# Performance work log

Hardware: AMD Instinct MI355X
Metric: run time of the kernel (lower is better)

The kernel has to match this reference:

```python
import jax, jax.numpy as jnp
import numpy as np

EMBED_DIM = 1024
NUM_HEADS = 16
HEAD_DIM = EMBED_DIM // NUM_HEADS
SCALE = float(np.sqrt(HEAD_DIM))
B, TQ, TK = 2, 2048, 2048


def setup_inputs() -> dict:
    key = jax.random.key(0)
    ks = jax.random.split(key, 16)
    s = 1.0 / np.sqrt(EMBED_DIM)
    inp = {
        "query": jax.random.normal(ks[0], (B, TQ, EMBED_DIM), jnp.float32),
        "key": jax.random.normal(ks[1], (B, TK, EMBED_DIM), jnp.float32),
        "value": jax.random.normal(ks[2], (B, TK, EMBED_DIM), jnp.float32),
        "key_padding_mask": jnp.zeros((B, TK), dtype=bool),
        "Wq": jax.random.uniform(ks[3], (EMBED_DIM, EMBED_DIM), jnp.float32, -s, s),
        "bq": jax.random.uniform(ks[4], (EMBED_DIM,), jnp.float32, -s, s),
        "Wk": jax.random.uniform(ks[5], (EMBED_DIM, EMBED_DIM), jnp.float32, -s, s),
        "bk": jax.random.uniform(ks[6], (EMBED_DIM,), jnp.float32, -s, s),
        "Wv": jax.random.uniform(ks[7], (EMBED_DIM, EMBED_DIM), jnp.float32, -s, s),
        "bv": jax.random.uniform(ks[8], (EMBED_DIM,), jnp.float32, -s, s),
        "Wo": jax.random.uniform(ks[9], (EMBED_DIM, EMBED_DIM), jnp.float32, -s, s),
        "bo": jax.random.uniform(ks[10], (EMBED_DIM,), jnp.float32, -s, s),
        "clr_bias_q": jax.random.normal(ks[11], (NUM_HEADS, 1, HEAD_DIM), jnp.float32) * 0.02,
        "clr_bias_k": jax.random.normal(ks[12], (NUM_HEADS, 1, HEAD_DIM), jnp.float32) * 0.02,
    }
    return inp


def reference(query, key, value, key_padding_mask, Wq, bq, Wk, bk, Wv, bv, Wo, bo,
              clr_bias_q, clr_bias_k):
    Bsz, Tq, _ = query.shape
    Tk = key.shape[1]

    def split_heads(x, W, b, T):
        # Linear (torch convention: x @ W.T + b) then [B, H, T, Dh]
        y = jnp.einsum('bte,fe->btf', x, W) + b
        return y.reshape(Bsz, T, NUM_HEADS, HEAD_DIM).transpose(0, 2, 1, 3)

    q = split_heads(query, Wq, bq, Tq)   # [B,H,Tq,Dh]
    k = split_heads(key, Wk, bk, Tk)     # [B,H,Tk,Dh]
    v = split_heads(value, Wv, bv, Tk)   # [B,H,Tk,Dh]

    # CLR centering + learned bias (Aitchison similarity)
    q_c = q - jnp.mean(q, axis=-1, keepdims=True) + clr_bias_q[None]
    k_c = k - jnp.mean(k, axis=-1, keepdims=True) + clr_bias_k[None]
    scores = jnp.einsum('bhqd,bhkd->bhqk', q_c, k_c) / SCALE  # [B,H,Tq,Tk]

    mask = key_padding_mask[:, None, None, :]  # [B,1,1,Tk], True = ignore
    scores = jnp.where(mask, -jnp.inf, scores)

    attn = jax.nn.softmax(scores, axis=-1)
    out = jnp.einsum('bhqk,bhkd->bhqd', attn, v)
    out = out.transpose(0, 2, 1, 3).reshape(Bsz, Tq, EMBED_DIM)
    return jnp.einsum('bte,fe->btf', out, Wo) + bo
```

## Files before the change

### kernel.cpp

```cpp
#include <hip/hip_runtime.h>
#include <stdint.h>

static constexpr int EMB   = 1024;
static constexpr int HEADS = 16;
static constexpr int HD    = 64;
static constexpr int BATCH = 2;
static constexpr int SEQ   = 2048;
static constexpr int BT    = BATCH * SEQ;
static constexpr float QSC = 0.18033688011112042f;

typedef short   short8  __attribute__((ext_vector_type(8)));
typedef float   float4v __attribute__((ext_vector_type(4)));

__device__ __forceinline__ ushort f2bf(float f) {
    union { float f; uint32_t i; } v; v.f = f;
    uint32_t x = v.i;
    return (ushort)((x + 0x7FFFu + ((x >> 16) & 1u)) >> 16);
}
__device__ __forceinline__ ushort f2bf_rn(float f) {
    union { float f; uint32_t i; } v; v.f = f;
    return (ushort)((v.i + 0x8000u) >> 16);
}
__device__ __forceinline__ uint32_t pack2bf(float lo, float hi) {
    union { float f; uint32_t u; } a, b; a.f = lo; b.f = hi;
    uint32_t ra = a.u + 0x7FFFu + ((a.u >> 16) & 1u);
    uint32_t rb = b.u + 0x7FFFu + ((b.u >> 16) & 1u);
    return (rb & 0xFFFF0000u) | (ra >> 16);
}
__device__ __forceinline__ float fast_exp2(float x) {
#if __has_builtin(__builtin_amdgcn_exp2f)
    return __builtin_amdgcn_exp2f(x);
#else
    return exp2f(x);
#endif
}

__device__ __forceinline__ void async_ld16(const void* g, void* l) {
    __builtin_amdgcn_global_load_lds(
        (const __attribute__((address_space(1))) void*)g,
        (__attribute__((address_space(3))) void*)l,
        16, 0, 0);
}

__global__ void cvt_all(const float* __restrict__ q, const float* __restrict__ k,
                        const float* __restrict__ v,
                        const float* __restrict__ wq, const float* __restrict__ wk,
                        const float* __restrict__ wv, const float* __restrict__ wo,
                        ushort* __restrict__ qb, ushort* __restrict__ kb,
                        ushort* __restrict__ vb,
                        ushort* __restrict__ wqb, ushort* __restrict__ wkb,
                        ushort* __restrict__ wvb, ushort* __restrict__ wob)
{
    int bid = blockIdx.x;
    const float* src; ushort* dst; size_t off;
    if (bid < 6144) {
        int seg = bid >> 11;
        src = seg == 0 ? q : (seg == 1 ? k : v);
        dst = seg == 0 ? qb : (seg == 1 ? kb : vb);
        off = (size_t)(bid & 2047) * 2048;
    } else {
        int t = bid - 6144, seg = t >> 9;
        src = seg == 0 ? wq : (seg == 1 ? wk : (seg == 2 ? wv : wo));
        dst = seg == 0 ? wqb : (seg == 1 ? wkb : (seg == 2 ? wvb : wob));
        off = (size_t)(t & 511) * 2048;
    }
    size_t base = off + (size_t)threadIdx.x * 8;
    float4 a0 = *(const float4*)(src + base);
    float4 a1 = *(const float4*)(src + base + 4);
    uint32_t o[4] = { pack2bf(a0.x, a0.y), pack2bf(a0.z, a0.w),
                      pack2bf(a1.x, a1.y), pack2bf(a1.z, a1.w) };
    *(uint4*)(dst + base) = *(uint4*)o;
}

__device__ __forceinline__ void gemm_core_128(
    const ushort* __restrict__ A, const ushort* __restrict__ W,
    int m0, int n0, int K,
    ushort* As, ushort* Ws,
    int wid, int lane, float4v acc[4][4])
{
    const int lrow8 = lane >> 3;
    const int gc    = (lane & 7) ^ lrow8;
    const ushort* Ab = A + (size_t)m0 * K + gc * 8;
    const ushort* Wb = W + (size_t)n0 * K + gc * 8;
    const int wm = (wid >> 1) * 64;
    const int wn = (wid & 1) * 64;

    for (int k0 = 0; k0 < K; k0 += 64) {
        __syncthreads();
#pragma unroll
        for (int it = 0; it < 4; ++it) {
            int rg = it * 4 + wid;
            int row = rg * 8 + lrow8;
            async_ld16(Ab + (size_t)row * K + k0, &As[rg * 512]);
            async_ld16(Wb + (size_t)row * K + k0, &Ws[rg * 512]);
        }
        __syncthreads();
#pragma unroll
        for (int ks = 0; ks < 2; ++ks) {
            const int c = ks * 4 + (lane >> 4);
            short8 af[4], wf[4];
#pragma unroll
            for (int i = 0; i < 4; i++) {
                int row = wm + i * 16 + (lane & 15);
                af[i] = *(const short8*)&As[row * 64 + ((c ^ (row & 7)) * 8)];
            }
#pragma unroll
            for (int j = 0; j < 4; j++) {
                int row = wn + j * 16 + (lane & 15);
                wf[j] = *(const short8*)&Ws[row * 64 + ((c ^ (row & 7)) * 8)];
            }
#pragma unroll
            for (int i = 0; i < 4; i++)
#pragma unroll
                for (int j = 0; j < 4; j++)
                    acc[i][j] = __builtin_amdgcn_mfma_f32_16x16x32_bf16(af[i], wf[j], acc[i][j], 0, 0, 0);
        }
    }
}

__global__ __launch_bounds__(256, 3)
void gemm_qkv(const ushort* __restrict__ qb, const ushort* __restrict__ kb,
              const ushort* __restrict__ vb,
              const ushort* __restrict__ wqb, const ushort* __restrict__ wkb,
              const ushort* __restrict__ wvb,
              const float* __restrict__ bq, const float* __restrict__ bk,
              const float* __restrict__ bv,
              const float* __restrict__ cbq, const float* __restrict__ cbk,
              ushort* __restrict__ qc, ushort* __restrict__ kc,
              ushort* __restrict__ vt)
{
    constexpr int SST = 136;
    __shared__ __align__(16) ushort S[128 * SST];

    const int z = blockIdx.z;
    const ushort* A    = z == 0 ? qb  : (z == 1 ? kb  : vb);
    const ushort* W    = z == 0 ? wqb : (z == 1 ? wkb : wvb);
    const float*  bias = z == 0 ? bq  : (z == 1 ? bk  : bv);
    const float*  clrb = z == 0 ? cbq : cbk;
    const float   scale = z == 0 ? QSC : 1.0f;

    const int tid  = threadIdx.x;
    const int wid  = tid >> 6;
    const int lane = tid & 63;
    const int m0 = blockIdx.y * 128;
    const int n0 = blockIdx.x * 128;
    const int wm = (wid >> 1) * 64;
    const int wn = (wid & 1) * 64;

    float4v acc[4][4];
#pragma unroll
    for (int i = 0; i < 4; i++)
#pragma unroll
        for (int j = 0; j < 4; j++) acc[i][j] = (float4v)0.0f;

    gemm_core_128(A, W, m0, n0, EMB, S, S + 128 * 64, wid, lane, acc);

    __syncthreads();

    const int h  = (n0 + wn) >> 6;
    const int ln = lane & 15;
#pragma unroll
    for (int i = 0; i < 4; i++) {
        float ys[4][4];
#pragma unroll
        for (int j = 0; j < 4; j++) {
            float bj = bias[n0 + wn + j * 16 + ln];
#pragma unroll
            for (int r = 0; r < 4; r++) ys[j][r] = acc[i][j][r] + bj;
        }
        const int lrow = wm + i * 16 + ((lane >> 4) << 2);

        if (z < 2) {
            float rs[4];
#pragma unroll
            for (int r = 0; r < 4; r++)
                rs[r] = ys[0][r] + ys[1][r] + ys[2][r] + ys[3][r];
#pragma unroll
            for (int r = 0; r < 4; r++)
#pragma unroll
                for (int off = 1; off < 16; off <<= 1)
                    rs[r] += __shfl_xor(rs[r], off, 64);
#pragma unroll
            for (int j = 0; j < 4; j++) {
                float cb = clrb[h * HD + ((wn + j * 16 + ln) & 63)];
#pragma unroll
                for (int r = 0; r < 4; r++)
                    S[(lrow + r) * SST + wn + j * 16 + ln] =
                        f2bf((ys[j][r] - rs[r] * (1.0f / 64.0f) + cb) * scale);
            }
        } else {
#pragma unroll
            for (int j = 0; j < 4; j++)
#pragma unroll
                for (int r = 0; r < 4; r++)
                    S[(wn + j * 16 + ln) * SST + lrow + r] = f2bf(ys[j][r]);
        }
    }
    __syncthreads();

    const int hbase = n0 >> 6;
    const int bloc  = m0 >> 11;
    const int tloc0 = m0 & (SEQ - 1);
    ushort* Yb = z == 0 ? qc : kc;
#pragma unroll
    for (int p = 0; p < 8; ++p) {
        int g = p * 256 + tid;
        int row = g >> 4, ch = g & 15;
        short8 val = *(const short8*)&S[row * SST + ch * 8];
        if (z < 2) {
            int gm = m0 + row;
            int bb = gm >> 11, tt = gm & (SEQ - 1);
            int hh = hbase + (ch >> 3);
            int d0 = (ch * 8) & 63;
            *(short8*)(Yb + (((size_t)(bb * HEADS + hh) * SEQ + tt) * HD + d0)) = val;
        } else {
            int nn = n0 + row;
            int hh = nn >> 6, dd = nn & 63;
            *(short8*)(vt + (((size_t)(bloc * HEADS + hh) * HD + dd) * SEQ
                             + tloc0 + ch * 8)) = val;
        }
    }
}

__global__ __launch_bounds__(256, 3)
void gemm_out(const ushort* __restrict__ A, const ushort* __restrict__ W,
              const float* __restrict__ bias, float* __restrict__ Y)
{
    __shared__ __align__(16) ushort As[128 * 64];
    __shared__ __align__(16) ushort Ws[128 * 64];

    const int tid  = threadIdx.x;
    const int wid  = tid >> 6;
    const int lane = tid & 63;
    const int m0 = blockIdx.y * 128;
    const int n0 = blockIdx.x * 128;
    const int wm = (wid >> 1) * 64;
    const int wn = (wid & 1) * 64;

    float4v acc[4][4];
#pragma unroll
    for (int i = 0; i < 4; i++)
#pragma unroll
        for (int j = 0; j < 4; j++) acc[i][j] = (float4v)0.0f;

    gemm_core_128(A, W, m0, n0, EMB, As, Ws, wid, lane, acc);

#pragma unroll
    for (int i = 0; i < 4; i++) {
        const int rowb = m0 + wm + i * 16 + ((lane >> 4) << 2);
#pragma unroll
        for (int j = 0; j < 4; j++) {
            int col = n0 + wn + j * 16 + (lane & 15);
            float bj = bias[col];
#pragma unroll
            for (int r = 0; r < 4; r++)
                Y[(size_t)(rowb + r) * EMB + col] = acc[i][j][r] + bj;
        }
    }
}

__global__ __launch_bounds__(256, 3)
void attn_kernel(const ushort* __restrict__ qc,
                 const ushort* __restrict__ kc,
                 const ushort* __restrict__ vt,
                 const unsigned char* __restrict__ mask,
                 ushort* __restrict__ out)
{
    __shared__ __align__(16) ushort Ks[128 * 64];
    __shared__ __align__(16) ushort Vs[64 * 128];
    __shared__ __align__(16) ushort Ps[4][16 * 136];

    const int tid  = threadIdx.x;
    const int wid  = tid >> 6;
    const int lane = tid & 63;

    const int bid = blockIdx.x;
    const int qt = bid & 31;
    const int h  = (bid >> 5) & 15;
    const int b  = bid >> 9;

    const ushort* qbase = qc + ((size_t)(b * HEADS + h)) * SEQ * HD;
    const ushort* kbase = kc + ((size_t)(b * HEADS + h)) * SEQ * HD;
    const ushort* vbase = vt + ((size_t)(b * HEADS + h)) * HD * SEQ;

    const int qrow = qt * 64 + wid * 16 + (lane & 15);
    short8 qf[2];
#pragma unroll
    for (int ks = 0; ks < 2; ++ks)
        qf[ks] = *(const short8*)(qbase + (size_t)qrow * HD + ks * 32 + (lane >> 4) * 8);

    float l_r[4] = {0.f, 0.f, 0.f, 0.f};
    float4v o[4];
#pragma unroll
    for (int j = 0; j < 4; j++) o[j] = (float4v)0.f;

    const int lrow8 = lane >> 3;
    const int gcK   = (lane & 7) ^ lrow8;
    ushort* Pw = &Ps[wid][0];

    for (int kt = 0; kt < SEQ / 128; ++kt) {
        __syncthreads();
#pragma unroll
        for (int it = 0; it < 4; ++it) {
            int row = (it * 4 + wid) * 8 + lrow8;
            async_ld16(kbase + (size_t)(kt * 128 + row) * HD + gcK * 8,
                       &Ks[(it * 4 + wid) * 512]);
        }
#pragma unroll
        for (int it = 0; it < 4; ++it) {
            int row = (it * 4 + wid) * 4 + (lane >> 4);
            int gc  = (lane & 15) ^ (row & 15);
            async_ld16(vbase + (size_t)row * SEQ + kt * 128 + gc * 8,
                       &Vs[(it * 4 + wid) * 512]);
        }
        __syncthreads();

        float4v s[8];
#pragma unroll
        for (int j = 0; j < 8; j++) {
            s[j] = (float4v)0.f;
#pragma unroll
            for (int ks = 0; ks < 2; ks++) {
                int row = j * 16 + (lane & 15);
                int c   = ks * 4 + (lane >> 4);
                short8 kf = *(const short8*)&Ks[row * 64 + ((c ^ (row & 7)) * 8)];
                s[j] = __builtin_amdgcn_mfma_f32_16x16x32_bf16(qf[ks], kf, s[j], 0, 0, 0);
            }
        }

#pragma unroll
        for (int j = 0; j < 8; j++) {
            int key = kt * 128 + j * 16 + (lane & 15);
            float mz = mask[b * SEQ + key] ? -1e30f : 0.0f;
            int prow = ((lane >> 4) << 2) * 136 + j * 16 + (lane & 15);
#pragma unroll
            for (int r = 0; r < 4; r++) {
                float p = fast_exp2(s[j][r] + mz);
                l_r[r] += p;
                Pw[prow + r * 136] = f2bf_rn(p);
            }
        }
        asm volatile("s_waitcnt lgkmcnt(0)" ::: "memory");

        short8 pf[4];
#pragma unroll
        for (int ks = 0; ks < 4; ks++)
            pf[ks] = *(const short8*)&Pw[(lane & 15) * 136 + ks * 32 + (lane >> 4) * 8];

#pragma unroll
        for (int j = 0; j < 4; j++) {
            int d = j * 16 + (lane & 15);
#pragma unroll
            for (int ks = 0; ks < 4; ks++) {
                int c = ks * 4 + (lane >> 4);
                short8 vf = *(const short8*)&Vs[d * 128 + ((c ^ (d & 15)) * 8)];
                o[j] = __builtin_amdgcn_mfma_f32_16x16x32_bf16(pf[ks], vf, o[j], 0, 0, 0);
            }
        }
    }

#pragma unroll
    for (int r = 0; r < 4; r++)
#pragma unroll
        for (int off = 1; off < 16; off <<= 1)
            l_r[r] += __shfl_xor(l_r[r], off, 64);

    const int qrow_out = qt * 64 + wid * 16 + ((lane >> 4) << 2);
#pragma unroll
    for (int j = 0; j < 4; j++) {
        int d = j * 16 + (lane & 15);
#pragma unroll
        for (int r = 0; r < 4; r++) {
            float val = o[j][r] / l_r[r];
            out[((size_t)(b * SEQ + qrow_out + r)) * EMB + h * HD + d] = f2bf(val);
        }
    }
}

extern "C" void kernel_launch(void* const* d_in, const int* in_sizes, int n_in,
                              void* d_out, int out_size, void* d_ws, size_t ws_size,
                              hipStream_t stream)
{
    const float* query = (const float*)d_in[0];
    const float* key_  = (const float*)d_in[1];
    const float* value = (const float*)d_in[2];
    const unsigned char* mask = (const unsigned char*)d_in[3];
    const float* Wq  = (const float*)d_in[4];
    const float* bq  = (const float*)d_in[5];
    const float* Wk  = (const float*)d_in[6];
    const float* bk  = (const float*)d_in[7];
    const float* Wv  = (const float*)d_in[8];
    const float* bv  = (const float*)d_in[9];
    const float* Wo  = (const float*)d_in[10];
    const float* bo  = (const float*)d_in[11];
    const float* cbq = (const float*)d_in[12];
    const float* cbk = (const float*)d_in[13];

    ushort* ws = (ushort*)d_ws;
    const size_t n1 = (size_t)BT * EMB;
    const size_t nw = (size_t)EMB * EMB;
    ushort* qb  = ws;
    ushort* kb  = qb  + n1;
    ushort* vb  = kb  + n1;
    ushort* wqb = vb  + n1;
    ushort* wkb = wqb + nw;
    ushort* wvb = wkb + nw;
    ushort* wob = wvb + nw;
    ushort* qc  = wob + nw;
    ushort* kc  = qc  + n1;
    ushort* vt  = kc  + n1;
    ushort* ao  = qb;

    cvt_all<<<8192, 256, 0, stream>>>(query, key_, value, Wq, Wk, Wv, Wo,
                                      qb, kb, vb, wqb, wkb, wvb, wob);

    dim3 gq(EMB / 128, BT / 128, 3);
    gemm_qkv<<<gq, 256, 0, stream>>>(qb, kb, vb, wqb, wkb, wvb,
                                     bq, bk, bv, cbq, cbk, qc, kc, vt);

    attn_kernel<<<BATCH * HEADS * (SEQ / 64), 256, 0, stream>>>(qc, kc, vt, mask, ao);

    dim3 go(EMB / 128, BT / 128);
    gemm_out<<<go, 256, 0, stream>>>(ao, wob, bo, (float*)d_out);
}
```

Before: 259.0 us.

## Write Q/K row-major, compute V^T via swapped GEMM, shrink out-proj tiles

The QKV projection now uses a flat 1D grid. Q and K are stored in plain [B*T, EMB] row-major layout, so each output tile is written contiguously, and the attention kernel indexes heads with an EMB stride. V is computed as W_v·V^T by swapping the GEMM operands, so the transposed V tile comes straight out of the MFMA layout and no longer needs a transposing LDS scatter. The output projection gets its own 64x128-tile GEMM loop with launch bounds of 2 and twice as many blocks, to improve CU fill. The risks are strided K/Q loads in attention and a lower occupancy hint on the output GEMM.

```diff
diff --git a/kernel.cpp b/kernel.cpp
--- a/kernel.cpp
+++ b/kernel.cpp
@@ -132,20 +132,22 @@
     constexpr int SST = 136;
     __shared__ __align__(16) ushort S[128 * SST];
 
-    const int z = blockIdx.z;
-    const ushort* A    = z == 0 ? qb  : (z == 1 ? kb  : vb);
-    const ushort* W    = z == 0 ? wqb : (z == 1 ? wkb : wvb);
-    const float*  bias = z == 0 ? bq  : (z == 1 ? bk  : bv);
-    const float*  clrb = z == 0 ? cbq : cbk;
-    const float   scale = z == 0 ? QSC : 1.0f;
+    const int bid = blockIdx.x;
+    const int z = bid >> 8;
+    const int r = bid & 255;
+    int m0, n0;
+    if (z < 2) { m0 = (r >> 3) * 128; n0 = (r & 7) * 128; }
+    else       { m0 = (r & 7) * 128;  n0 = (r >> 3) * 128; }
+
+    const ushort* A = z == 0 ? qb  : (z == 1 ? kb  : wvb);
+    const ushort* W = z == 0 ? wqb : (z == 1 ? wkb : vb);
 
     const int tid  = threadIdx.x;
     const int wid  = tid >> 6;
     const int lane = tid & 63;
-    const int m0 = blockIdx.y * 128;
-    const int n0 = blockIdx.x * 128;
     const int wm = (wid >> 1) * 64;
     const int wn = (wid & 1) * 64;
+    const int ln = lane & 15;
 
     float4v acc[4][4];
 #pragma unroll
@@ -157,104 +159,147 @@
 
     __syncthreads();
 
-    const int h  = (n0 + wn) >> 6;
-    const int ln = lane & 15;
-#pragma unroll
-    for (int i = 0; i < 4; i++) {
-        float ys[4][4];
-#pragma unroll
-        for (int j = 0; j < 4; j++) {
-            float bj = bias[n0 + wn + j * 16 + ln];
-#pragma unroll
-            for (int r = 0; r < 4; r++) ys[j][r] = acc[i][j][r] + bj;
-        }
-        const int lrow = wm + i * 16 + ((lane >> 4) << 2);
-
-        if (z < 2) {
+    if (z < 2) {
+        const float* bias = z == 0 ? bq : bk;
+        const float* clrb = z == 0 ? cbq : cbk;
+        const float  scale = z == 0 ? QSC : 1.0f;
+        const int h = (n0 + wn) >> 6;
+#pragma unroll
+        for (int i = 0; i < 4; i++) {
+            float ys[4][4];
+#pragma unroll
+            for (int j = 0; j < 4; j++) {
+                float bj = bias[n0 + wn + j * 16 + ln];
+#pragma unroll
+                for (int rr = 0; rr < 4; rr++) ys[j][rr] = acc[i][j][rr] + bj;
+            }
+            const int lrow = wm + i * 16 + ((lane >> 4) << 2);
             float rs[4];
 #pragma unroll
-            for (int r = 0; r < 4; r++)
-                rs[r] = ys[0][r] + ys[1][r] + ys[2][r] + ys[3][r];
-#pragma unroll
-            for (int r = 0; r < 4; r++)
+            for (int rr = 0; rr < 4; rr++)
+                rs[rr] = ys[0][rr] + ys[1][rr] + ys[2][rr] + ys[3][rr];
+#pragma unroll
+            for (int rr = 0; rr < 4; rr++)
 #pragma unroll
                 for (int off = 1; off < 16; off <<= 1)
-                    rs[r] += __shfl_xor(rs[r], off, 64);
+                    rs[rr] += __shfl_xor(rs[rr], off, 64);
 #pragma unroll
             for (int j = 0; j < 4; j++) {
                 float cb = clrb[h * HD + ((wn + j * 16 + ln) & 63)];
 #pragma unroll
-                for (int r = 0; r < 4; r++)
-                    S[(lrow + r) * SST + wn + j * 16 + ln] =
-                        f2bf((ys[j][r] - rs[r] * (1.0f / 64.0f) + cb) * scale);
-            }
-        } else {
+                for (int rr = 0; rr < 4; rr++)
+                    S[(lrow + rr) * SST + wn + j * 16 + ln] =
+                        f2bf((ys[j][rr] - rs[rr] * (1.0f / 64.0f) + cb) * scale);
+            }
+        }
+    } else {
+#pragma unroll
+        for (int i = 0; i < 4; i++) {
+            const int lrow = wm + i * 16 + ((lane >> 4) << 2);
+            float bvr[4];
+#pragma unroll
+            for (int rr = 0; rr < 4; rr++) bvr[rr] = bv[m0 + lrow + rr];
 #pragma unroll
             for (int j = 0; j < 4; j++)
 #pragma unroll
-                for (int r = 0; r < 4; r++)
-                    S[(wn + j * 16 + ln) * SST + lrow + r] = f2bf(ys[j][r]);
+                for (int rr = 0; rr < 4; rr++)
+                    S[(lrow + rr) * SST + wn + j * 16 + ln] =
+                        f2bf(acc[i][j][rr] + bvr[rr]);
         }
     }
     __syncthreads();
 
-    const int hbase = n0 >> 6;
-    const int bloc  = m0 >> 11;
-    const int tloc0 = m0 & (SEQ - 1);
-    ushort* Yb = z == 0 ? qc : kc;
+    ushort* Yb = z == 0 ? qc : (z == 1 ? kc : vt);
 #pragma unroll
     for (int p = 0; p < 8; ++p) {
         int g = p * 256 + tid;
         int row = g >> 4, ch = g & 15;
         short8 val = *(const short8*)&S[row * SST + ch * 8];
         if (z < 2) {
-            int gm = m0 + row;
-            int bb = gm >> 11, tt = gm & (SEQ - 1);
-            int hh = hbase + (ch >> 3);
-            int d0 = (ch * 8) & 63;
-            *(short8*)(Yb + (((size_t)(bb * HEADS + hh) * SEQ + tt) * HD + d0)) = val;
+            *(short8*)(Yb + (size_t)(m0 + row) * EMB + n0 + ch * 8) = val;
         } else {
-            int nn = n0 + row;
-            int hh = nn >> 6, dd = nn & 63;
-            *(short8*)(vt + (((size_t)(bloc * HEADS + hh) * HD + dd) * SEQ
-                             + tloc0 + ch * 8)) = val;
-        }
-    }
-}
-
-__global__ __launch_bounds__(256, 3)
+            int e = m0 + row;
+            int ng = n0 + ch * 8;
+            int bb = ng >> 11, tt = ng & (SEQ - 1);
+            int hh = e >> 6, dd = e & 63;
+            *(short8*)(Yb + ((size_t)(bb * HEADS + hh) * HD + dd) * SEQ + tt) = val;
+        }
+    }
+}
+
+__global__ __launch_bounds__(256, 2)
 void gemm_out(const ushort* __restrict__ A, const ushort* __restrict__ W,
               const float* __restrict__ bias, float* __restrict__ Y)
 {
-    __shared__ __align__(16) ushort As[128 * 64];
+    __shared__ __align__(16) ushort As[64 * 64];
     __shared__ __align__(16) ushort Ws[128 * 64];
 
     const int tid  = threadIdx.x;
     const int wid  = tid >> 6;
     const int lane = tid & 63;
-    const int m0 = blockIdx.y * 128;
+    const int m0 = blockIdx.y * 64;
     const int n0 = blockIdx.x * 128;
-    const int wm = (wid >> 1) * 64;
+    const int wm = (wid >> 1) * 32;
     const int wn = (wid & 1) * 64;
 
-    float4v acc[4][4];
-#pragma unroll
-    for (int i = 0; i < 4; i++)
+    float4v acc[2][4];
+#pragma unroll
+    for (int i = 0; i < 2; i++)
 #pragma unroll
         for (int j = 0; j < 4; j++) acc[i][j] = (float4v)0.0f;
 
-    gemm_core_128(A, W, m0, n0, EMB, As, Ws, wid, lane, acc);
-
-#pragma unroll
-    for (int i = 0; i < 4; i++) {
+    const int lrow8 = lane >> 3;
+    const int gc    = (lane & 7) ^ lrow8;
+    const ushort* Ab = A + (size_t)m0 * EMB + gc * 8;
+    const ushort* Wb = W + (size_t)n0 * EMB + gc * 8;
+
+    for (int k0 = 0; k0 < EMB; k0 += 64) {
+        __syncthreads();
+#pragma unroll
+        for (int it = 0; it < 6; ++it) {
+            int rg = it * 4 + wid;
+            if (rg < 8) {
+                int row = rg * 8 + lrow8;
+                async_ld16(Ab + (size_t)row * EMB + k0, &As[rg * 512]);
+            } else {
+                int wg = rg - 8;
+                int row = wg * 8 + lrow8;
+                async_ld16(Wb + (size_t)row * EMB + k0, &Ws[wg * 512]);
+            }
+        }
+        __syncthreads();
+#pragma unroll
+        for (int ks = 0; ks < 2; ++ks) {
+            const int c = ks * 4 + (lane >> 4);
+            short8 af[2], wf[4];
+#pragma unroll
+            for (int i = 0; i < 2; i++) {
+                int row = wm + i * 16 + (lane & 15);
+                af[i] = *(const short8*)&As[row * 64 + ((c ^ (row & 7)) * 8)];
+            }
+#pragma unroll
+            for (int j = 0; j < 4; j++) {
+                int row = wn + j * 16 + (lane & 15);
+                wf[j] = *(const short8*)&Ws[row * 64 + ((c ^ (row & 7)) * 8)];
+            }
+#pragma unroll
+            for (int i = 0; i < 2; i++)
+#pragma unroll
+                for (int j = 0; j < 4; j++)
+                    acc[i][j] = __builtin_amdgcn_mfma_f32_16x16x32_bf16(af[i], wf[j], acc[i][j], 0, 0, 0);
+        }
+    }
+
+#pragma unroll
+    for (int i = 0; i < 2; i++) {
         const int rowb = m0 + wm + i * 16 + ((lane >> 4) << 2);
 #pragma unroll
         for (int j = 0; j < 4; j++) {
             int col = n0 + wn + j * 16 + (lane & 15);
             float bj = bias[col];
 #pragma unroll
-            for (int r = 0; r < 4; r++)
-                Y[(size_t)(rowb + r) * EMB + col] = acc[i][j][r] + bj;
+            for (int rr = 0; rr < 4; rr++)
+                Y[(size_t)(rowb + rr) * EMB + col] = acc[i][j][rr] + bj;
         }
     }
 }
@@ -279,15 +324,14 @@
     const int h  = (bid >> 5) & 15;
     const int b  = bid >> 9;
 
-    const ushort* qbase = qc + ((size_t)(b * HEADS + h)) * SEQ * HD;
-    const ushort* kbase = kc + ((size_t)(b * HEADS + h)) * SEQ * HD;
     const ushort* vbase = vt + ((size_t)(b * HEADS + h)) * HD * SEQ;
 
     const int qrow = qt * 64 + wid * 16 + (lane & 15);
     short8 qf[2];
 #pragma unroll
     for (int ks = 0; ks < 2; ++ks)
-        qf[ks] = *(const short8*)(qbase + (size_t)qrow * HD + ks * 32 + (lane >> 4) * 8);
+        qf[ks] = *(const short8*)(qc + (size_t)(b * SEQ + qrow) * EMB
+                                  + h * HD + ks * 32 + (lane >> 4) * 8);
 
     float l_r[4] = {0.f, 0.f, 0.f, 0.f};
     float4v o[4];
@@ -303,7 +347,7 @@
 #pragma unroll
         for (int it = 0; it < 4; ++it) {
             int row = (it * 4 + wid) * 8 + lrow8;
-            async_ld16(kbase + (size_t)(kt * 128 + row) * HD + gcK * 8,
+            async_ld16(kc + (size_t)(b * SEQ + kt * 128 + row) * EMB + h * HD + gcK * 8,
                        &Ks[(it * 4 + wid) * 512]);
         }
 #pragma unroll
@@ -334,10 +378,10 @@
             float mz = mask[b * SEQ + key] ? -1e30f : 0.0f;
             int prow = ((lane >> 4) << 2) * 136 + j * 16 + (lane & 15);
 #pragma unroll
-            for (int r = 0; r < 4; r++) {
-                float p = fast_exp2(s[j][r] + mz);
-                l_r[r] += p;
-                Pw[prow + r * 136] = f2bf_rn(p);
+            for (int rr = 0; rr < 4; rr++) {
+                float p = fast_exp2(s[j][rr] + mz);
+                l_r[rr] += p;
+                Pw[prow + rr * 136] = f2bf_rn(p);
             }
         }
         asm volatile("s_waitcnt lgkmcnt(0)" ::: "memory");
@@ -360,19 +404,19 @@
     }
 
 #pragma unroll
-    for (int r = 0; r < 4; r++)
+    for (int rr = 0; rr < 4; rr++)
 #pragma unroll
         for (int off = 1; off < 16; off <<= 1)
-            l_r[r] += __shfl_xor(l_r[r], off, 64);
+            l_r[rr] += __shfl_xor(l_r[rr], off, 64);
 
     const int qrow_out = qt * 64 + wid * 16 + ((lane >> 4) << 2);
 #pragma unroll
     for (int j = 0; j < 4; j++) {
         int d = j * 16 + (lane & 15);
 #pragma unroll
-        for (int r = 0; r < 4; r++) {
-            float val = o[j][r] / l_r[r];
-            out[((size_t)(b * SEQ + qrow_out + r)) * EMB + h * HD + d] = f2bf(val);
+        for (int rr = 0; rr < 4; rr++) {
+            float val = o[j][rr] / l_r[rr];
+            out[((size_t)(b * SEQ + qrow_out + rr)) * EMB + h * HD + d] = f2bf(val);
         }
     }
 }
@@ -414,12 +458,11 @@
     cvt_all<<<8192, 256, 0, stream>>>(query, key_, value, Wq, Wk, Wv, Wo,
                                       qb, kb, vb, wqb, wkb, wvb, wob);
 
-    dim3 gq(EMB / 128, BT / 128, 3);
-    gemm_qkv<<<gq, 256, 0, stream>>>(qb, kb, vb, wqb, wkb, wvb,
-                                     bq, bk, bv, cbq, cbk, qc, kc, vt);
+    gemm_qkv<<<768, 256, 0, stream>>>(qb, kb, vb, wqb, wkb, wvb,
+                                      bq, bk, bv, cbq, cbk, qc, kc, vt);
 
     attn_kernel<<<BATCH * HEADS * (SEQ / 64), 256, 0, stream>>>(qc, kc, vt, mask, ao);
 
-    dim3 go(EMB / 128, BT / 128);
+    dim3 go(EMB / 128, BT / 64);
     gemm_out<<<go, 256, 0, stream>>>(ao, wob, bo, (float*)d_out);
 }
```

After: 251.0 us. 3.1% less time.
